# Optimization experiments

Measured on AMD Instinct MI355X. Metric: run time of the kernel, lower is better.

Reference implementation:

```python
import jax, jax.numpy as jnp
import numpy as np

B, S, D, L = 32, 4096, 1024, 1

def setup_inputs() -> dict:
    key = jax.random.key(0)
    ks = jax.random.split(key, 9)
    sc = 1.0 / np.sqrt(D)
    return {
        "encoder_outputs": jax.random.normal(ks[0], (B, S, D), jnp.float32),
        "decoder_hidden_state": jax.random.normal(ks[1], (L, B, D), jnp.float32),
        "attn_mask": jax.random.randint(ks[2], (B, S), 0, 2) > 0,
        "Wa_w": jax.random.normal(ks[3], (D, D), jnp.float32) * sc,
        "Wa_b": jax.random.normal(ks[4], (D,), jnp.float32) * sc,
        "Ua_w": jax.random.normal(ks[5], (D, D), jnp.float32) * sc,
        "Ua_b": jax.random.normal(ks[6], (D,), jnp.float32) * sc,
        "Va_w": jax.random.normal(ks[7], (1, D), jnp.float32) * sc,
        "Va_b": jax.random.normal(ks[8], (1,), jnp.float32) * sc,
    }

def reference(encoder_outputs, decoder_hidden_state, attn_mask,
              Wa_w, Wa_b, Ua_w, Ua_b, Va_w, Va_b):
    # Ua(decoder_hidden_state): [L,B,D] -> transpose(0,1) -> [B,L,D] -> keep layer 0 -> [B,1,D]
    dec = jnp.einsum('lbd,ed->lbe', decoder_hidden_state, Ua_w) + Ua_b
    dec = jnp.transpose(dec, (1, 0, 2))[:, 0:1, :]            # [B,1,D]
    # Wa(encoder_outputs): [B,S,D]
    enc = jnp.einsum('bsd,ed->bse', encoder_outputs, Wa_w) + Wa_b
    # scores = Va(tanh(enc + dec)) -> [B,S,1] -> [B,1,S]
    scores = jnp.einsum('bsd,od->bso', jnp.tanh(enc + dec), Va_w) + Va_b
    scores = scores[:, :, 0][:, None, :]                      # [B,1,S]
    scores = jnp.where(attn_mask[:, None, :], scores, -jnp.inf)
    weights = jax.nn.softmax(scores, axis=-1)
    return weights
```

## Files before the change

kernel.cpp:

```cpp
#include <hip/hip_runtime.h>
#include <math.h>

#define D_DIM 1024
#define S_DIM 4096
#define B_DIM 32
#define M_TOTAL (B_DIM * S_DIM)

#define KQ   128
#define NPH  8

using short8 = __attribute__((ext_vector_type(8))) short;
using f32x4  = __attribute__((ext_vector_type(4))) float;

static __device__ __forceinline__ unsigned short f2bf(float x) {
    unsigned int u = __float_as_uint(x);
    u += 0x7fffu + ((u >> 16) & 1u);
    return (unsigned short)(u >> 16);
}

static __device__ __forceinline__ float fast_tanh(float x) {
    float e2 = __expf(2.0f * x);
    return 1.0f - 2.0f * __builtin_amdgcn_rcpf(e2 + 1.0f);
}

__global__ __launch_bounds__(256) void mask_detect_kernel(
        const unsigned int* __restrict__ m, int* __restrict__ flag) {
    __shared__ unsigned int red[4];
    int t = threadIdx.x;
    unsigned int acc = 0;
    for (int i = t; i < 32768; i += 256) acc |= (m[i] & 0xFFFFFF00u);
    #pragma unroll
    for (int k = 1; k <= 32; k <<= 1) acc |= __shfl_xor(acc, k, 64);
    if ((t & 63) == 0) red[t >> 6] = acc;
    __syncthreads();
    if (t == 0) flag[0] = ((red[0] | red[1] | red[2] | red[3]) != 0) ? 1 : 0;
}

__global__ __launch_bounds__(256) void wconv_kernel(
        const float* __restrict__ W, unsigned short* __restrict__ Wt) {
    int tid  = blockIdx.x * 256 + threadIdx.x;
    int lane = tid & 63;
    int kc   = (tid >> 6) & 31;
    int et   = tid >> 11;
    int e = et * 16 + (lane & 15);
    int k = kc * 32 + (lane >> 4) * 8;
    const float* src = W + (size_t)e * D_DIM + k;
    float4 v0 = *(const float4*)(src);
    float4 v1 = *(const float4*)(src + 4);
    short8 pk;
    pk[0] = (short)f2bf(v0.x); pk[1] = (short)f2bf(v0.y);
    pk[2] = (short)f2bf(v0.z); pk[3] = (short)f2bf(v0.w);
    pk[4] = (short)f2bf(v1.x); pk[5] = (short)f2bf(v1.y);
    pk[6] = (short)f2bf(v1.z); pk[7] = (short)f2bf(v1.w);
    *(short8*)(Wt + (size_t)tid * 8) = pk;
}

__global__ __launch_bounds__(256) void off_kernel(
        const float* __restrict__ h, const float* __restrict__ Uw,
        const float* __restrict__ Ub, const float* __restrict__ Wab,
        float* __restrict__ off) {
    int wg   = blockIdx.x * 4 + (threadIdx.x >> 6);
    int lane = threadIdx.x & 63;
    int b = wg >> 10, e = wg & 1023;
    const float4* h4 = (const float4*)(h + (size_t)b * D_DIM);
    const float4* u4 = (const float4*)(Uw + (size_t)e * D_DIM);
    float s = 0.f;
    #pragma unroll
    for (int c = 0; c < 4; ++c) {
        float4 a = h4[c * 64 + lane];
        float4 w = u4[c * 64 + lane];
        s += a.x * w.x + a.y * w.y + a.z * w.z + a.w * w.w;
    }
    #pragma unroll
    for (int m = 32; m; m >>= 1) s += __shfl_xor(s, m, 64);
    if (lane == 0) off[b * D_DIM + e] = s + Ub[e] + Wab[e];
}

__global__ __launch_bounds__(512, 4) void score_kernel(
        const float* __restrict__ A,
        const unsigned short* __restrict__ Wt,
        const float* __restrict__ off,
        const float* __restrict__ Va,
        float* __restrict__ scores)
{
    __shared__ short As[2][64 * KQ];
    __shared__ float score_lds[64];

    const int bid  = blockIdx.x;
    const int pr   = (bid & 7) * 256 + ((bid >> 3) >> 1);
    const int h    = (bid >> 3) & 1;
    const int row0 = pr * 64;
    const int b    = row0 >> 12;

    const int t = threadIdx.x;
    if (t < 64) score_lds[t] = 0.f;

    const int wave = t >> 6, lane = t & 63;
    const int l15 = lane & 15, lhi = lane >> 4;
    const int e0 = h * 512 + wave * 64;

    const unsigned short* WtB =
        Wt + ((size_t)(h * 32 + wave * 4) * 32) * 512 + (size_t)lane * 8;

    const int sr = t >> 3;
    const int sk = (t & 7) * 16;
    const float* Asrc = A + (size_t)(row0 + sr) * D_DIM + sk;
    const int swz   = (sr & 7) << 3;
    const int sidx0 = sr * KQ + (sk ^ swz);
    const int sidx1 = sr * KQ + ((sk + 8) ^ swz);

    f32x4 acc[4][4];
    #pragma unroll
    for (int rf = 0; rf < 4; ++rf)
        #pragma unroll
        for (int cf = 0; cf < 4; ++cf) acc[rf][cf] = (f32x4){0.f, 0.f, 0.f, 0.f};

    {
        float4 v0 = *(const float4*)(Asrc + 0);
        float4 v1 = *(const float4*)(Asrc + 4);
        float4 v2 = *(const float4*)(Asrc + 8);
        float4 v3 = *(const float4*)(Asrc + 12);
        short8 pk0, pk1;
        pk0[0] = (short)f2bf(v0.x); pk0[1] = (short)f2bf(v0.y);
        pk0[2] = (short)f2bf(v0.z); pk0[3] = (short)f2bf(v0.w);
        pk0[4] = (short)f2bf(v1.x); pk0[5] = (short)f2bf(v1.y);
        pk0[6] = (short)f2bf(v1.z); pk0[7] = (short)f2bf(v1.w);
        pk1[0] = (short)f2bf(v2.x); pk1[1] = (short)f2bf(v2.y);
        pk1[2] = (short)f2bf(v2.z); pk1[3] = (short)f2bf(v2.w);
        pk1[4] = (short)f2bf(v3.x); pk1[5] = (short)f2bf(v3.y);
        pk1[6] = (short)f2bf(v3.z); pk1[7] = (short)f2bf(v3.w);
        *(short8*)(&As[0][sidx0]) = pk0;
        *(short8*)(&As[0][sidx1]) = pk1;
    }
    __syncthreads();

    for (int q = 0; q < NPH; ++q) {
        const int cur = q & 1;

        float4 p0, p1, p2, p3;
        if (q < NPH - 1) {
            const float* nx = Asrc + (q + 1) * KQ;
            p0 = *(const float4*)(nx + 0);
            p1 = *(const float4*)(nx + 4);
            p2 = *(const float4*)(nx + 8);
            p3 = *(const float4*)(nx + 12);
        }

        #pragma unroll
        for (int kk = 0; kk < KQ / 32; ++kk) {
            const int k0 = kk * 32 + lhi * 8;
            const int kglob = q * 4 + kk;
            short8 af[4];
            #pragma unroll
            for (int rf = 0; rf < 4; ++rf) {
                int row = rf * 16 + l15;
                af[rf] = *(const short8*)(&As[cur][row * KQ + (k0 ^ ((row & 7) << 3))]);
            }
            __builtin_amdgcn_s_setprio(1);
            #pragma unroll
            for (int cf = 0; cf < 4; ++cf) {
                short8 bfr = *(const short8*)(WtB + (size_t)(cf * 32 + kglob) * 512);
                #pragma unroll
                for (int rf = 0; rf < 4; ++rf)
                    acc[rf][cf] = __builtin_amdgcn_mfma_f32_16x16x32_bf16(
                        af[rf], bfr, acc[rf][cf], 0, 0, 0);
            }
            __builtin_amdgcn_s_setprio(0);
        }

        if (q < NPH - 1) {
            short8 pk0, pk1;
            pk0[0] = (short)f2bf(p0.x); pk0[1] = (short)f2bf(p0.y);
            pk0[2] = (short)f2bf(p0.z); pk0[3] = (short)f2bf(p0.w);
            pk0[4] = (short)f2bf(p1.x); pk0[5] = (short)f2bf(p1.y);
            pk0[6] = (short)f2bf(p1.z); pk0[7] = (short)f2bf(p1.w);
            pk1[0] = (short)f2bf(p2.x); pk1[1] = (short)f2bf(p2.y);
            pk1[2] = (short)f2bf(p2.z); pk1[3] = (short)f2bf(p2.w);
            pk1[4] = (short)f2bf(p3.x); pk1[5] = (short)f2bf(p3.y);
            pk1[6] = (short)f2bf(p3.z); pk1[7] = (short)f2bf(p3.w);
            *(short8*)(&As[cur ^ 1][sidx0]) = pk0;
            *(short8*)(&As[cur ^ 1][sidx1]) = pk1;
        }
        __syncthreads();
    }

    float sp[4][4];
    #pragma unroll
    for (int rf = 0; rf < 4; ++rf)
        #pragma unroll
        for (int j = 0; j < 4; ++j) sp[rf][j] = 0.f;

    #pragma unroll
    for (int cf = 0; cf < 4; ++cf) {
        int e = e0 + cf * 16 + l15;
        float offv = off[b * D_DIM + e];
        float vav  = Va[e];
        #pragma unroll
        for (int rf = 0; rf < 4; ++rf)
            #pragma unroll
            for (int j = 0; j < 4; ++j) {
                float x = acc[rf][cf][j] + offv;
                sp[rf][j] += fast_tanh(x) * vav;
            }
    }

    #pragma unroll
    for (int rf = 0; rf < 4; ++rf)
        #pragma unroll
        for (int j = 0; j < 4; ++j) {
            float v = sp[rf][j];
            v += __shfl_xor(v, 1, 64);
            v += __shfl_xor(v, 2, 64);
            v += __shfl_xor(v, 4, 64);
            v += __shfl_xor(v, 8, 64);
            if (l15 == 0) atomicAdd(&score_lds[rf * 16 + lhi * 4 + j], v);
        }
    __syncthreads();

    if (t < 64) scores[(size_t)h * M_TOTAL + row0 + t] = score_lds[t];
}

__global__ __launch_bounds__(256) void softmax_kernel(
        const float* __restrict__ scores, const void* __restrict__ mask,
        const int* __restrict__ flag, float* __restrict__ out) {
    __shared__ float red[4];
    const int b = blockIdx.x, t = threadIdx.x;
    const float* s0 = scores + (size_t)b * S_DIM;
    const float* s1 = scores + (size_t)M_TOTAL + (size_t)b * S_DIM;
    const int mode8 = flag[0];

    float v[16];
    float mx = -INFINITY;
    if (mode8) {
        const unsigned char* m = (const unsigned char*)mask + (size_t)b * S_DIM;
        #pragma unroll
        for (int i = 0; i < 16; ++i) {
            int idx = i * 256 + t;
            v[i] = m[idx] ? (s0[idx] + s1[idx]) : -INFINITY;
            mx = fmaxf(mx, v[i]);
        }
    } else {
        const int* m = (const int*)mask + (size_t)b * S_DIM;
        #pragma unroll
        for (int i = 0; i < 16; ++i) {
            int idx = i * 256 + t;
            v[i] = m[idx] ? (s0[idx] + s1[idx]) : -INFINITY;
            mx = fmaxf(mx, v[i]);
        }
    }
    #pragma unroll
    for (int k = 1; k <= 32; k <<= 1) mx = fmaxf(mx, __shfl_xor(mx, k, 64));
    if ((t & 63) == 0) red[t >> 6] = mx;
    __syncthreads();
    mx = fmaxf(fmaxf(red[0], red[1]), fmaxf(red[2], red[3]));
    __syncthreads();

    float sum = 0.f;
    #pragma unroll
    for (int i = 0; i < 16; ++i) {
        v[i] = __expf(v[i] - mx);
        sum += v[i];
    }
    #pragma unroll
    for (int k = 1; k <= 32; k <<= 1) sum += __shfl_xor(sum, k, 64);
    if ((t & 63) == 0) red[t >> 6] = sum;
    __syncthreads();
    sum = red[0] + red[1] + red[2] + red[3];
    float inv = 1.f / sum;
    #pragma unroll
    for (int i = 0; i < 16; ++i) out[(size_t)b * S_DIM + i * 256 + t] = v[i] * inv;
}

extern "C" void kernel_launch(void* const* d_in, const int* in_sizes, int n_in,
                              void* d_out, int out_size, void* d_ws, size_t ws_size,
                              hipStream_t stream) {
    const float* enc  = (const float*)d_in[0];
    const float* dech = (const float*)d_in[1];
    const void*  mask = d_in[2];
    const float* Wa_w = (const float*)d_in[3];
    const float* Wa_b = (const float*)d_in[4];
    const float* Ua_w = (const float*)d_in[5];
    const float* Ua_b = (const float*)d_in[6];
    const float* Va_w = (const float*)d_in[7];
    float* out = (float*)d_out;

    char* ws = (char*)d_ws;
    unsigned short* Wt = (unsigned short*)ws;
    float* off    = (float*)(ws + (1u << 21));
    float* scores = (float*)(ws + (1u << 21) + (1u << 17));
    int*   flag   = (int*)(ws + (1u << 21) + (1u << 17) + (1u << 20));

    hipLaunchKernelGGL(mask_detect_kernel, dim3(1), dim3(256), 0, stream,
                       (const unsigned int*)mask, flag);
    hipLaunchKernelGGL(wconv_kernel, dim3(512), dim3(256), 0, stream, Wa_w, Wt);
    hipLaunchKernelGGL(off_kernel, dim3(8192), dim3(256), 0, stream,
                       dech, Ua_w, Ua_b, Wa_b, off);
    hipLaunchKernelGGL(score_kernel, dim3(4096), dim3(512), 0, stream,
                       enc, Wt, off, Va_w, scores);
    hipLaunchKernelGGL(softmax_kernel, dim3(B_DIM), dim3(256), 0, stream,
                       scores, mask, flag, out);
}
```

Before: 379.7 us.

## Stage fp32 A tiles via direct global-to-LDS loads and prefetch B fragments

Replaces the register-staged load of fp32 A tiles (global load, convert to bf16, store to LDS) with global_load_lds DMA into an fp32 LDS buffer, followed by a cooperative in-LDS conversion to a swizzled bf16 buffer. The weight layout is reordered so each k-step's B fragments are contiguous, and B fragments are double-buffered in registers with a one-step prefetch. Barriers and waitcnts are hand-placed. The aim is to cut register pressure and VGPR round trips and to overlap global loads with MFMA work, at the cost of an extra LDS pass, more LDS use and fragile manual synchronisation.

After: 397.3 us. +4.6%, slower.

```diff
diff --git a/kernel.cpp b/kernel.cpp
--- a/kernel.cpp
+++ b/kernel.cpp
@@ -1,4 +1,5 @@
 #include <hip/hip_runtime.h>
+#include <hip/hip_bf16.h>
 #include <math.h>
 
 #define D_DIM 1024
@@ -12,10 +13,18 @@
 using short8 = __attribute__((ext_vector_type(8))) short;
 using f32x4  = __attribute__((ext_vector_type(4))) float;
 
+#define AS3 __attribute__((address_space(3)))
+#define AS1 __attribute__((address_space(1)))
+
 static __device__ __forceinline__ unsigned short f2bf(float x) {
     unsigned int u = __float_as_uint(x);
     u += 0x7fffu + ((u >> 16) & 1u);
     return (unsigned short)(u >> 16);
+}
+
+static __device__ __forceinline__ unsigned int pk2(float lo, float hi) {
+    __hip_bfloat162 h = __float22bfloat162_rn(float2{lo, hi});
+    unsigned int u; __builtin_memcpy(&u, &h, 4); return u;
 }
 
 static __device__ __forceinline__ float fast_tanh(float x) {
@@ -38,12 +47,12 @@
 
 __global__ __launch_bounds__(256) void wconv_kernel(
         const float* __restrict__ W, unsigned short* __restrict__ Wt) {
-    int tid  = blockIdx.x * 256 + threadIdx.x;
-    int lane = tid & 63;
-    int kc   = (tid >> 6) & 31;
-    int et   = tid >> 11;
-    int e = et * 16 + (lane & 15);
-    int k = kc * 32 + (lane >> 4) * 8;
+    int tid   = blockIdx.x * 256 + threadIdx.x;
+    int lane  = tid & 63;
+    int c     = (tid >> 6) & 63;
+    int kglob = tid >> 12;
+    int e = c * 16 + (lane & 15);
+    int k = kglob * 32 + (lane >> 4) * 8;
     const float* src = W + (size_t)e * D_DIM + k;
     float4 v0 = *(const float4*)(src);
     float4 v1 = *(const float4*)(src + 4);
@@ -83,7 +92,8 @@
         const float* __restrict__ Va,
         float* __restrict__ scores)
 {
-    __shared__ short As[2][64 * KQ];
+    __shared__ float          fbuf[64 * KQ];
+    __shared__ unsigned short bbuf[64 * KQ];
     __shared__ float score_lds[64];
 
     const int bid  = blockIdx.x;
@@ -98,16 +108,12 @@
     const int wave = t >> 6, lane = t & 63;
     const int l15 = lane & 15, lhi = lane >> 4;
     const int e0 = h * 512 + wave * 64;
-
-    const unsigned short* WtB =
-        Wt + ((size_t)(h * 32 + wave * 4) * 32) * 512 + (size_t)lane * 8;
-
-    const int sr = t >> 3;
-    const int sk = (t & 7) * 16;
-    const float* Asrc = A + (size_t)(row0 + sr) * D_DIM + sk;
-    const int swz   = (sr & 7) << 3;
-    const int sidx0 = sr * KQ + (sk ^ swz);
-    const int sidx1 = sr * KQ + ((sk + 8) ^ swz);
+    const int c0 = h * 32 + wave * 4;
+
+    const unsigned short* Bp = Wt + (size_t)c0 * 512 + (size_t)lane * 8;
+
+    const int srow = wave * 8 + (lane >> 5);
+    const int scol = (lane & 31) * 4;
 
     f32x4 acc[4][4];
     #pragma unroll
@@ -115,73 +121,75 @@
         #pragma unroll
         for (int cf = 0; cf < 4; ++cf) acc[rf][cf] = (f32x4){0.f, 0.f, 0.f, 0.f};
 
-    {
-        float4 v0 = *(const float4*)(Asrc + 0);
-        float4 v1 = *(const float4*)(Asrc + 4);
-        float4 v2 = *(const float4*)(Asrc + 8);
-        float4 v3 = *(const float4*)(Asrc + 12);
-        short8 pk0, pk1;
-        pk0[0] = (short)f2bf(v0.x); pk0[1] = (short)f2bf(v0.y);
-        pk0[2] = (short)f2bf(v0.z); pk0[3] = (short)f2bf(v0.w);
-        pk0[4] = (short)f2bf(v1.x); pk0[5] = (short)f2bf(v1.y);
-        pk0[6] = (short)f2bf(v1.z); pk0[7] = (short)f2bf(v1.w);
-        pk1[0] = (short)f2bf(v2.x); pk1[1] = (short)f2bf(v2.y);
-        pk1[2] = (short)f2bf(v2.z); pk1[3] = (short)f2bf(v2.w);
-        pk1[4] = (short)f2bf(v3.x); pk1[5] = (short)f2bf(v3.y);
-        pk1[6] = (short)f2bf(v3.z); pk1[7] = (short)f2bf(v3.w);
-        *(short8*)(&As[0][sidx0]) = pk0;
-        *(short8*)(&As[0][sidx1]) = pk1;
-    }
-    __syncthreads();
+    short8 bA[4], bB[4];
+
+    #define STAGE(Q)                                                          \
+        _Pragma("unroll")                                                     \
+        for (int i = 0; i < 4; ++i) {                                         \
+            int row = srow + i * 2;                                           \
+            const float* gsrc = A + (size_t)(row0 + row) * D_DIM + (Q) * KQ   \
+                              + (scol ^ ((row & 7) << 3));                    \
+            __builtin_amdgcn_global_load_lds(                                 \
+                (const AS1 float*)gsrc,                                       \
+                (AS3 float*)&fbuf[(wave * 8 + i * 2) * KQ], 16, 0, 0);        \
+        }
+
+    #define LOADB(dst, kg)                                                    \
+        _Pragma("unroll")                                                     \
+        for (int cf = 0; cf < 4; ++cf)                                        \
+            dst[cf] = *(const short8*)(Bp + ((size_t)(kg) * 64 + cf) * 512);
+
+    STAGE(0);
+    LOADB(bA, 0);
+    asm volatile("s_waitcnt vmcnt(4)" ::: "memory");
+    __builtin_amdgcn_s_barrier();
 
     for (int q = 0; q < NPH; ++q) {
-        const int cur = q & 1;
-
-        float4 p0, p1, p2, p3;
-        if (q < NPH - 1) {
-            const float* nx = Asrc + (q + 1) * KQ;
-            p0 = *(const float4*)(nx + 0);
-            p1 = *(const float4*)(nx + 4);
-            p2 = *(const float4*)(nx + 8);
-            p3 = *(const float4*)(nx + 12);
-        }
-
-        #pragma unroll
-        for (int kk = 0; kk < KQ / 32; ++kk) {
+        #pragma unroll
+        for (int j = 0; j < 2; ++j) {
+            int kkc = (wave & 1) * 2 + j;
+            int row = (wave >> 1) * 16 + l15;
+            int k   = kkc * 32 + lhi * 8;
+            int fidx = row * KQ + (k ^ ((row & 7) << 3));
+            float4 fa = *(const float4*)&fbuf[fidx];
+            float4 fb = *(const float4*)&fbuf[fidx + 4];
+            uint4 o;
+            o.x = pk2(fa.x, fa.y); o.y = pk2(fa.z, fa.w);
+            o.z = pk2(fb.x, fb.y); o.w = pk2(fb.z, fb.w);
+            *(uint4*)((char*)bbuf + row * 256 + ((k * 2) ^ ((row & 7) << 4))) = o;
+        }
+        asm volatile("s_waitcnt lgkmcnt(0)" ::: "memory");
+        __builtin_amdgcn_s_barrier();
+
+        if (q < NPH - 1) STAGE(q + 1);
+
+        #pragma unroll
+        for (int kk = 0; kk < 4; ++kk) {
+            const int kg = q * 4 + kk;
+            short8* use = (kk & 1) ? bB : bA;
+            short8* pre = (kk & 1) ? bA : bB;
+            if (kg + 1 < 32) { LOADB(pre, kg + 1); }
+
+            short8 af[4];
             const int k0 = kk * 32 + lhi * 8;
-            const int kglob = q * 4 + kk;
-            short8 af[4];
             #pragma unroll
             for (int rf = 0; rf < 4; ++rf) {
                 int row = rf * 16 + l15;
-                af[rf] = *(const short8*)(&As[cur][row * KQ + (k0 ^ ((row & 7) << 3))]);
+                af[rf] = *(const short8*)((const char*)bbuf + row * 256
+                                          + ((k0 * 2) ^ ((row & 7) << 4)));
             }
             __builtin_amdgcn_s_setprio(1);
             #pragma unroll
-            for (int cf = 0; cf < 4; ++cf) {
-                short8 bfr = *(const short8*)(WtB + (size_t)(cf * 32 + kglob) * 512);
+            for (int rf = 0; rf < 4; ++rf)
                 #pragma unroll
-                for (int rf = 0; rf < 4; ++rf)
+                for (int cf = 0; cf < 4; ++cf)
                     acc[rf][cf] = __builtin_amdgcn_mfma_f32_16x16x32_bf16(
-                        af[rf], bfr, acc[rf][cf], 0, 0, 0);
-            }
+                        af[rf], use[cf], acc[rf][cf], 0, 0, 0);
             __builtin_amdgcn_s_setprio(0);
         }
 
-        if (q < NPH - 1) {
-            short8 pk0, pk1;
-            pk0[0] = (short)f2bf(p0.x); pk0[1] = (short)f2bf(p0.y);
-            pk0[2] = (short)f2bf(p0.z); pk0[3] = (short)f2bf(p0.w);
-            pk0[4] = (short)f2bf(p1.x); pk0[5] = (short)f2bf(p1.y);
-            pk0[6] = (short)f2bf(p1.z); pk0[7] = (short)f2bf(p1.w);
-            pk1[0] = (short)f2bf(p2.x); pk1[1] = (short)f2bf(p2.y);
-            pk1[2] = (short)f2bf(p2.z); pk1[3] = (short)f2bf(p2.w);
-            pk1[4] = (short)f2bf(p3.x); pk1[5] = (short)f2bf(p3.y);
-            pk1[6] = (short)f2bf(p3.z); pk1[7] = (short)f2bf(p3.w);
-            *(short8*)(&As[cur ^ 1][sidx0]) = pk0;
-            *(short8*)(&As[cur ^ 1][sidx1]) = pk1;
-        }
-        __syncthreads();
+        if (q < NPH - 1) asm volatile("s_waitcnt vmcnt(4)" ::: "memory");
+        __builtin_amdgcn_s_barrier();
     }
 
     float sp[4][4];
```
